# Kernel optimization log

Measured on AMD Instinct MI355X. Metric: run time of the kernel, lower is better.

The kernel has to match this reference:

```python
import jax, jax.numpy as jnp
import numpy as np

B, S, H, W, E, NH = 8, 16, 32, 32, 128, 8
HD = E // NH
EPS = 1e-5


def setup_inputs() -> dict:
    key = jax.random.key(0)
    ks = jax.random.split(key, 6)
    sc = lambda fan: 1.0 / np.sqrt(fan).astype(np.float32)
    return {
        "inputs": jax.random.normal(ks[0], (B, S, H, W, E), jnp.float32),
        "W_proj": jax.random.normal(ks[1], (E, E), jnp.float32) * sc(E),
        "ln_gamma": jnp.ones((E,), jnp.float32),
        "ln_beta": jnp.zeros((E,), jnp.float32),
        "W_in": jax.random.normal(ks[2], (E, 3 * E), jnp.float32) * sc(E),
        "W_out": jax.random.normal(ks[3], (E, E), jnp.float32) * sc(E),
        "conv_k": jax.random.normal(ks[4], (4 * E, 2 * E, 3, 3), jnp.float32) * sc(2 * E * 9),
    }


def reference(inputs, W_proj, ln_gamma, ln_beta, W_in, W_out, conv_k):
    # x = silu(project(inputs))
    x = jax.nn.silu(inputs @ W_proj)
    # LayerNorm over last dim
    mu = x.mean(-1, keepdims=True)
    var = x.var(-1, keepdims=True)
    x = (x - mu) * jax.lax.rsqrt(var + EPS) * ln_gamma + ln_beta
    # Multi-head attention over the sequence dim, batched over (b, h, w)
    qkv = (x @ W_in).reshape(B, S, H, W, NH, 3 * HD)
    q, k, v = jnp.split(qkv, 3, axis=-1)
    scale = 1.0 / np.sqrt(HD).astype(np.float32)
    scores = jnp.einsum('bshwid,blhwid->bhwisl', q, k) * scale  # (B,H,W,NH,S,S)
    tril = jnp.tril(jnp.ones((S, S), jnp.float32))
    # faithful to source: +1.0 on/below diagonal, -1000.0 above
    mask = tril * 1.0 + (1.0 - tril) * (-1000.0)
    attnw = jax.nn.softmax(scores + mask, axis=-1)
    ao = jnp.einsum('bhwisl,blhwid->bshwid', attnw, v).reshape(B, S, H, W, E)
    x = ao @ W_out + inputs  # residual
    # ConvLSTM over seq: (B,S,H,W,E) -> (S,B,E,H,W) for scan
    xc = jnp.transpose(x, (1, 0, 4, 2, 3))
    h0 = jnp.zeros((B, E, H, W), x.dtype)
    c0 = jnp.zeros((B, E, H, W), x.dtype)

    def step(carry, xt):
        h, c = carry
        comb = jnp.concatenate([xt, h], axis=1)  # (B, 2E, H, W)
        cc = jax.lax.conv_general_dilated(
            comb, conv_k, window_strides=(1, 1), padding='SAME',
            dimension_numbers=('NCHW', 'OIHW', 'NCHW'))
        ci, cf, co, cg = jnp.split(cc, 4, axis=1)
        c_next = jax.nn.sigmoid(cf) * c + jax.nn.sigmoid(ci) * jnp.tanh(cg)
        h_next = jax.nn.sigmoid(co) * jnp.tanh(c_next)
        return (h_next, c_next), h_next

    _, outs = jax.lax.scan(step, (h0, c0), xc)  # (S,B,E,H,W)
    return jnp.transpose(outs, (1, 0, 3, 4, 2))  # (B,S,H,W,E)
```

## Files before the change

### kernel.cpp

```cpp
#include <hip/hip_runtime.h>
#include <math.h>

#define B_  8
#define S_  16
#define H_  32
#define W_  32
#define E_  128
#define NH_ 8
#define HD_ 16
#define HW_ (H_*W_)
#define NTOK (B_*S_*H_*W_)

typedef __attribute__((ext_vector_type(8))) short short8;
typedef __attribute__((ext_vector_type(4))) short short4v;
typedef __attribute__((ext_vector_type(4))) float floatx4;

__device__ __forceinline__ float sigf(float x){
    return 1.f/(1.f+__expf(-x));
}
__device__ __forceinline__ float tanh_fast(float x){
    x = fminf(fmaxf(x, -15.f), 15.f);
    float e = __expf(2.f*x);
    return (e-1.f)/(e+1.f);
}
__device__ __forceinline__ unsigned short f2bf(float f){
    unsigned int u = __float_as_uint(f);
    u = (u + 0x7fffu + ((u >> 16) & 1u)) >> 16;
    return (unsigned short)u;
}
__device__ __forceinline__ float bf2f(unsigned short h){
    return __uint_as_float(((unsigned int)h) << 16);
}

__device__ __forceinline__ void st_gate(float* p, float v){ *p = v; }
__device__ __forceinline__ void st_gate(unsigned short* p, float v){ *p = f2bf(v); }
__device__ __forceinline__ void load_gate(const float* p, float* o){
    float4 v = *(const float4*)p; o[0]=v.x; o[1]=v.y; o[2]=v.z; o[3]=v.w;
}
__device__ __forceinline__ void load_gate(const unsigned short* p, float* o){
    ushort4 v = *(const ushort4*)p;
    o[0]=bf2f(v.x); o[1]=bf2f(v.y); o[2]=bf2f(v.z); o[3]=bf2f(v.w);
}

__global__ __launch_bounds__(256)
void k_pack_wproj(const float* __restrict__ Wp, short* __restrict__ Wpp){
    int p = blockIdx.x*256 + threadIdx.x;
    int L = p & 63;
    int idx = p >> 6;
    int nt = idx / 12, kb = idx - nt*12;
    int n = nt*16 + (L & 15);
    int kr = (kb & 3)*32 + (L >> 4)*8;
    bool lo = (kb >= 8);
    short8 v;
    #pragma unroll
    for (int j=0;j<8;j++){
        float wv = Wp[(kr+j)*128 + n];
        unsigned short h = f2bf(wv);
        v[j] = lo ? (short)f2bf(wv - bf2f(h)) : (short)h;
    }
    *(short8*)&Wpp[(long)p*8] = v;
}

__global__ __launch_bounds__(256,2)
void k_proj_ln_mfma(const float* __restrict__ in, const short* __restrict__ Wpp,
                    const float* __restrict__ gamma, const float* __restrict__ beta,
                    float* __restrict__ X){
    __shared__ short As[64*264];
    int tid = threadIdx.x;
    int w = tid >> 6, L = tid & 63;
    int quad = L >> 4, lm = L & 15;
    long r0 = (long)blockIdx.x * 64;

    {
        int c = (tid & 31)*4;
        int rbase = tid >> 5;
        #pragma unroll
        for (int rr=0; rr<8; rr++){
            int r = rr*8 + rbase;
            float4 v = *(const float4*)&in[(r0 + r)*128 + c];
            short4v hv, lv;
            unsigned short h;
            h = f2bf(v.x); hv[0]=(short)h; lv[0]=(short)f2bf(v.x - bf2f(h));
            h = f2bf(v.y); hv[1]=(short)h; lv[1]=(short)f2bf(v.y - bf2f(h));
            h = f2bf(v.z); hv[2]=(short)h; lv[2]=(short)f2bf(v.z - bf2f(h));
            h = f2bf(v.w); hv[3]=(short)h; lv[3]=(short)f2bf(v.w - bf2f(h));
            *(short4v*)&As[r*264 + c] = hv;
            *(short4v*)&As[r*264 + 128 + c] = lv;
        }
    }
    __syncthreads();

    floatx4 acc[8];
    #pragma unroll
    for (int nt=0;nt<8;nt++) acc[nt] = (floatx4){0.f,0.f,0.f,0.f};
    const short8* Bp8 = (const short8*)Wpp;
    int arow = (w*16 + lm)*264 + quad*8;
    #pragma unroll
    for (int kb=0; kb<12; kb++){
        int off = (kb<4) ? kb*32 : ((kb<8) ? 128+(kb-4)*32 : (kb-8)*32);
        short8 af = *(const short8*)&As[arow + off];
        #pragma unroll
        for (int nt=0;nt<8;nt++){
            short8 bf = Bp8[(nt*12+kb)*64 + L];
            acc[nt] = __builtin_amdgcn_mfma_f32_16x16x32_bf16(af, bf, acc[nt], 0,0,0);
        }
    }

    float g[8], bb[8];
    #pragma unroll
    for (int nt=0;nt<8;nt++){ g[nt]=gamma[nt*16+lm]; bb[nt]=beta[nt*16+lm]; }
    float s1[4]={0,0,0,0}, s2[4]={0,0,0,0};
    #pragma unroll
    for (int nt=0;nt<8;nt++)
        #pragma unroll
        for (int r=0;r<4;r++){
            float a = acc[nt][r];
            float si = a*sigf(a);
            acc[nt][r] = si;
            s1[r] += si; s2[r] += si*si;
        }
    #pragma unroll
    for (int d=1; d<16; d<<=1)
        #pragma unroll
        for (int r=0;r<4;r++){
            s1[r] += __shfl_xor(s1[r], d);
            s2[r] += __shfl_xor(s2[r], d);
        }
    float mu[4], rs[4];
    #pragma unroll
    for (int r=0;r<4;r++){
        mu[r] = s1[r]*(1.f/128.f);
        float var = s2[r]*(1.f/128.f) - mu[r]*mu[r];
        rs[r] = rsqrtf(var + 1e-5f);
    }
    #pragma unroll
    for (int nt=0;nt<8;nt++)
        #pragma unroll
        for (int r=0;r<4;r++){
            long row = r0 + w*16 + quad*4 + r;
            X[row*128 + nt*16 + lm] = (acc[nt][r]-mu[r])*rs[r]*g[nt] + bb[nt];
        }
}

__global__ __launch_bounds__(256)
void k_pack_win(const float* __restrict__ Win, short* __restrict__ Winp){
    int p = blockIdx.x*256 + threadIdx.x;
    int L = p & 63;
    int idx = p >> 6;
    int nt = idx >> 2, kc = idx & 3;
    int n = nt*16 + (L & 15);
    int k0 = kc*32 + (L >> 4)*8;
    short8 v;
    #pragma unroll
    for (int j=0;j<8;j++) v[j] = (short)f2bf(Win[(k0+j)*384 + n]);
    *(short8*)&Winp[(long)p*8] = v;
}

__global__ __launch_bounds__(256)
void k_pack_wout(const float* __restrict__ Wout, short* __restrict__ Woutp){
    int p = blockIdx.x*256 + threadIdx.x;
    int L = p & 63;
    int idx = p >> 6;
    int h = idx >> 3, nt = idx & 7;
    int n = nt*16 + (L & 15);
    int k0 = (L >> 4)*8;
    short8 v;
    #pragma unroll
    for (int j=0;j<8;j++){
        int k = k0 + j;
        v[j] = (k < 16) ? (short)f2bf(Wout[(h*16+k)*128 + n]) : (short)0;
    }
    *(short8*)&Woutp[(long)p*8] = v;
}

__global__ __launch_bounds__(256,5)
void k_attn_mfma(const float* __restrict__ X, const short* __restrict__ Winp,
                 const short* __restrict__ Woutp, const float* __restrict__ resid,
                 float* __restrict__ Y){
    __shared__ short lds[16000];
    const int XO=0;
    const int QO=8704;
    const int KO=10240;
    const int VO=11776;
    const int PO=12928;
    const int AOO=14464;
    int tid = threadIdx.x;
    int w = tid >> 6, L = tid & 63;
    int quad = L >> 4, lm = L & 15;
    int b = blockIdx.x >> 8, tile = blockIdx.x & 255;
    int hw0 = tile * 4;
    int hw = hw0 + w;

    {
        int cq = L & 31, rh = L >> 5;
        for (int p=0; p<8; p++){
            int m = w*16 + p*2 + rh;
            int s = m & 15;
            float4 v = *(const float4*)&X[((((long)b*16 + s)*1024) + hw)*128 + cq*4];
            short4v hv;
            hv[0]=(short)f2bf(v.x); hv[1]=(short)f2bf(v.y);
            hv[2]=(short)f2bf(v.z); hv[3]=(short)f2bf(v.w);
            *(short4v*)&lds[XO + m*136 + cq*4] = hv;
        }
    }

    floatx4 Oa[8];
    #pragma unroll
    for (int nt=0;nt<8;nt++) Oa[nt] = (floatx4){0.f,0.f,0.f,0.f};

    const floatx4 zc = (floatx4){0.f,0.f,0.f,0.f};
    const short8 z8 = {0,0,0,0,0,0,0,0};
    int m0 = w*16;

    for (int h=0; h<8; h++){
        floatx4 qacc[3];
        #pragma unroll
        for (int t=0;t<3;t++) qacc[t] = zc;
        #pragma unroll
        for (int kc=0;kc<4;kc++){
            short8 af = *(const short8*)&lds[XO + (m0+lm)*136 + kc*32 + quad*8];
            #pragma unroll
            for (int t=0;t<3;t++){
                int nt = 3*h + t;
                short8 bf = *(const short8*)&Winp[(long)((nt*4+kc)*64 + L)*8];
                qacc[t] = __builtin_amdgcn_mfma_f32_16x16x32_bf16(af, bf, qacc[t], 0,0,0);
            }
        }
        #pragma unroll
        for (int r=0;r<4;r++){
            lds[QO + (m0+quad*4+r)*24 + lm] = (short)f2bf(qacc[0][r]);
            lds[KO + (m0+quad*4+r)*24 + lm] = (short)f2bf(qacc[1][r]);
        }
        {
            short4v vv;
            #pragma unroll
            for (int r=0;r<4;r++) vv[r] = (short)f2bf(qacc[2][r]);
            *(short4v*)&lds[VO + lm*72 + m0 + quad*4] = vv;
        }

        {
            short8 qf = z8, kf = z8;
            if (quad < 2){
                qf = *(const short8*)&lds[QO + (m0+lm)*24 + quad*8];
                kf = *(const short8*)&lds[KO + (m0+lm)*24 + quad*8];
            }
            floatx4 scv = __builtin_amdgcn_mfma_f32_16x16x32_bf16(qf, kf, zc, 0,0,0);
            float pv[4], mr[4];
            #pragma unroll
            for (int r=0;r<4;r++){
                int si = quad*4 + r;
                pv[r] = scv[r]*0.25f + (lm <= si ? 1.0f : -1000.0f);
                mr[r] = pv[r];
            }
            #pragma unroll
            for (int d=1; d<16; d<<=1)
                #pragma unroll
                for (int r=0;r<4;r++) mr[r] = fmaxf(mr[r], __shfl_xor(mr[r], d));
            float ex[4], sm[4];
            #pragma unroll
            for (int r=0;r<4;r++){ ex[r] = __expf(pv[r]-mr[r]); sm[r] = ex[r]; }
            #pragma unroll
            for (int d=1; d<16; d<<=1)
                #pragma unroll
                for (int r=0;r<4;r++) sm[r] += __shfl_xor(sm[r], d);
            #pragma unroll
            for (int r=0;r<4;r++)
                lds[PO + (m0+quad*4+r)*24 + lm] = (short)f2bf(ex[r]/sm[r]);

            short8 pf = z8, vf = z8;
            if (quad < 2){
                pf = *(const short8*)&lds[PO + (m0+lm)*24 + quad*8];
                vf = *(const short8*)&lds[VO + lm*72 + m0 + quad*8];
            }
            floatx4 aov = __builtin_amdgcn_mfma_f32_16x16x32_bf16(pf, vf, zc, 0,0,0);
            #pragma unroll
            for (int r=0;r<4;r++)
                lds[AOO + (m0+quad*4+r)*24 + lm] = (short)f2bf(aov[r]);
        }

        {
            short8 aof = z8;
            if (quad < 2)
                aof = *(const short8*)&lds[AOO + (m0+lm)*24 + quad*8];
            #pragma unroll
            for (int nt=0;nt<8;nt++){
                short8 wf = *(const short8*)&Woutp[(long)((h*8+nt)*64 + L)*8];
                Oa[nt] = __builtin_amdgcn_mfma_f32_16x16x32_bf16(aof, wf, Oa[nt], 0,0,0);
            }
        }
    }

    #pragma unroll
    for (int nt=0;nt<8;nt++){
        int n = nt*16 + lm;
        #pragma unroll
        for (int r=0;r<4;r++){
            int s = quad*4 + r;
            long addr = (((long)b*16 + s)*1024 + hw)*128 + n;
            Y[addr] = Oa[nt][r] + resid[addr];
        }
    }
}

__global__ __launch_bounds__(256)
void k_pack_w(const float* __restrict__ ck, short* __restrict__ Bp){
    int p = blockIdx.x*256 + threadIdx.x;
    int L = p & 63;
    int nt = (p >> 6) & 31;
    int c32 = (p >> 11) & 7;
    int tap = p >> 14;
    int oc = nt*16 + (L & 15);
    int kq = L >> 4;
    short8 v;
    #pragma unroll
    for (int j=0;j<8;j++){
        int ic = c32*32 + kq*8 + j;
        v[j] = (short)f2bf(ck[(oc*256+ic)*9 + tap]);
    }
    *(short8*)&Bp[(long)p*8] = v;
}

__global__ __launch_bounds__(256)
void k_pack_x(const float* __restrict__ X, short* __restrict__ xh, int s, int zero_h){
    int idx = blockIdx.x*256 + threadIdx.x;
    int row = idx >> 4;
    int ch = (idx & 15) * 8;
    int b = row >> 10, hw = row & 1023;
    const float* src = X + (((long)(b*16+s)*1024 + hw)*128 + ch);
    float4 a = *(const float4*)src;
    float4 c = *(const float4*)(src+4);
    short8 v;
    v[0]=(short)f2bf(a.x); v[1]=(short)f2bf(a.y); v[2]=(short)f2bf(a.z); v[3]=(short)f2bf(a.w);
    v[4]=(short)f2bf(c.x); v[5]=(short)f2bf(c.y); v[6]=(short)f2bf(c.z); v[7]=(short)f2bf(c.w);
    *(short8*)&xh[(long)row*256 + ch] = v;
    if (zero_h){
        short8 z = {0,0,0,0,0,0,0,0};
        *(short8*)&xh[(long)row*256 + 128 + ch] = z;
    }
}

template<typename GT>
__global__ __launch_bounds__(512,2)
void k_conv_mfma(const short* __restrict__ xh, const short* __restrict__ Bp,
                 GT* __restrict__ gbuf){
    __shared__ short As[4*34*264];
    int tid = threadIdx.x;
    int Nblk = blockIdx.x & 1, g = blockIdx.x >> 1;
    int b = g >> 4, y0 = (g & 15)*2;
    int w = tid >> 6, L = tid & 63;
    int quad = L >> 4, lm = L & 15;
    int wm = w >> 2, wn = w & 3;
    int ntg = Nblk*16 + wn*4;

    const short8 z8 = {0,0,0,0,0,0,0,0};
    {
        short8 vs[9];
        #pragma unroll
        for (int i=0; i<9; i++){
            int pidx = i*512 + tid;
            short8 v = z8;
            if (pidx < 4352){
                int cb  = pidx & 31;
                int pos = pidx >> 5;
                int row = pos / 34;
                int xp  = pos - row*34;
                int yy = y0 - 1 + row, xx = xp - 1;
                if (yy>=0 && yy<32 && xx>=0 && xx<32)
                    v = *(const short8*)&xh[(((long)(b*32+yy)*32+xx)<<8) + cb*8];
            }
            vs[i] = v;
        }
        #pragma unroll
        for (int i=0; i<9; i++){
            int pidx = i*512 + tid;
            if (pidx < 4352){
                int cb  = pidx & 31;
                int pos = pidx >> 5;
                *(short8*)&As[pos*264 + cb*8] = vs[i];
            }
        }
    }
    __syncthreads();

    floatx4 acc[2][4];
    #pragma unroll
    for (int mtl=0;mtl<2;mtl++)
        #pragma unroll
        for (int nti=0;nti<4;nti++)
            acc[mtl][nti] = (floatx4){0.f,0.f,0.f,0.f};

    const short8* Bp8 = (const short8*)Bp;

    for (int tap=0; tap<9; tap++){
        int dy = tap/3 - 1, dx = tap - (tap/3)*3 - 1;
        int abase[2];
        #pragma unroll
        for (int mtl=0;mtl<2;mtl++){
            int x = mtl*16 + lm;
            abase[mtl] = (((wm+dy+1)*34) + x + dx + 1)*264 + quad*8;
        }
        #pragma unroll
        for (int sic=0; sic<4; sic++){
            #pragma unroll
            for (int c2=0; c2<2; c2++){
                short8 bfr[4];
                #pragma unroll
                for (int nti=0;nti<4;nti++)
                    bfr[nti] = Bp8[((tap*8 + sic*2 + c2)*32 + ntg + nti)*64 + L];
                #pragma unroll
                for (int mtl=0;mtl<2;mtl++){
                    short8 afr = *(const short8*)&As[abase[mtl] + sic*64 + c2*32];
                    #pragma unroll
                    for (int nti=0;nti<4;nti++)
                        acc[mtl][nti] = __builtin_amdgcn_mfma_f32_16x16x32_bf16(afr, bfr[nti], acc[mtl][nti], 0,0,0);
                }
            }
        }
    }

    #pragma unroll
    for (int mtl=0;mtl<2;mtl++){
        #pragma unroll
        for (int nti=0;nti<4;nti++){
            int n = Nblk*256 + (wn*4+nti)*16 + lm;
            #pragma unroll
            for (int r=0;r<4;r++){
                long row = (long)g*64 + (wm*2+mtl)*16 + quad*4 + r;
                st_gate(&gbuf[row*512 + n], acc[mtl][nti][r]);
            }
        }
    }
}

template<typename GT>
__global__ __launch_bounds__(256)
void k_lstm(const GT* __restrict__ gbuf, float* __restrict__ cbuf,
            float* __restrict__ X, short* __restrict__ xh, int s){
    int idx = blockIdx.x*256 + threadIdx.x;
    int row = idx >> 5;
    int c4 = (idx & 31)*4;
    float gi[4], gf[4], go[4], gg[4];
    const GT* gp = gbuf + (long)row*512 + c4;
    load_gate(gp,       gi);
    load_gate(gp + 128, gf);
    load_gate(gp + 256, go);
    load_gate(gp + 384, gg);
    float co[4];
    if (s == 0){ co[0]=co[1]=co[2]=co[3]=0.f; }
    else {
        float4 cv = *(const float4*)&cbuf[(long)row*128 + c4];
        co[0]=cv.x; co[1]=cv.y; co[2]=cv.z; co[3]=cv.w;
    }
    float cn[4], hn[4];
    #pragma unroll
    for (int j=0;j<4;j++){
        cn[j] = sigf(gf[j])*co[j] + sigf(gi[j])*tanh_fast(gg[j]);
        hn[j] = sigf(go[j])*tanh_fast(cn[j]);
    }
    *(float4*)&cbuf[(long)row*128 + c4] = make_float4(cn[0],cn[1],cn[2],cn[3]);
    int b = row >> 10, hw = row & 1023;
    long xoff = (((long)(b*16+s)*1024 + hw)*128) + c4;
    *(float4*)&X[xoff] = make_float4(hn[0],hn[1],hn[2],hn[3]);
    ushort4 hv;
    hv.x = f2bf(hn[0]); hv.y = f2bf(hn[1]); hv.z = f2bf(hn[2]); hv.w = f2bf(hn[3]);
    *(ushort4*)&xh[(long)row*256 + 128 + c4] = hv;
    if (s < 15){
        long x2 = (((long)(b*16+s+1)*1024 + hw)*128) + c4;
        float4 xv = *(const float4*)&X[x2];
        ushort4 xb;
        xb.x = f2bf(xv.x); xb.y = f2bf(xv.y); xb.z = f2bf(xv.z); xb.w = f2bf(xv.w);
        *(ushort4*)&xh[(long)row*256 + c4] = xb;
    }
}

extern "C" void kernel_launch(void* const* d_in, const int* in_sizes, int n_in,
                              void* d_out, int out_size, void* d_ws, size_t ws_size,
                              hipStream_t stream){
    const float* inputs = (const float*)d_in[0];
    const float* Wp     = (const float*)d_in[1];
    const float* gamma  = (const float*)d_in[2];
    const float* beta   = (const float*)d_in[3];
    const float* Win    = (const float*)d_in[4];
    const float* Wout   = (const float*)d_in[5];
    const float* ck     = (const float*)d_in[6];
    float* X = (float*)d_out;

    char* ws = (char*)d_ws;
    const size_t szB    = 147456ull*16;
    const size_t szXH   = 8192ull*256*2;
    const size_t szC    = 8192ull*128*4;
    const size_t szWin  = 6144ull*16;
    const size_t szWout = 4096ull*16;
    short* Bp    = (short*)(ws);
    short* xh    = (short*)(ws + szB);
    float* cbuf  = (float*)(ws + szB + szXH);
    short* Winp  = (short*)(ws + szB + szXH + szC);
    short* Woutp = (short*)(ws + szB + szXH + szC + szWin);
    char*  gch   =         ws + szB + szXH + szC + szWin + szWout;
    bool gate_f32 = ws_size >= (szB + szXH + szC + szWin + szWout + 8192ull*512*4);
    short* Wprojp = (short*)gch;

    k_pack_w<<<576, 256, 0, stream>>>(ck, Bp);
    k_pack_win<<<24, 256, 0, stream>>>(Win, Winp);
    k_pack_wout<<<16, 256, 0, stream>>>(Wout, Woutp);
    k_pack_wproj<<<24, 256, 0, stream>>>(Wp, Wprojp);
    k_proj_ln_mfma<<<NTOK/64, 256, 0, stream>>>(inputs, Wprojp, gamma, beta, X);
    k_attn_mfma<<<2048, 256, 0, stream>>>(X, Winp, Woutp, inputs, X);
    k_pack_x<<<512, 256, 0, stream>>>(X, xh, 0, 1);

    if (gate_f32){
        float* gbuf = (float*)gch;
        for (int s=0; s<16; s++){
            k_conv_mfma<float><<<256, 512, 0, stream>>>(xh, Bp, gbuf);
            k_lstm<float><<<1024, 256, 0, stream>>>(gbuf, cbuf, X, xh, s);
        }
    } else {
        unsigned short* gbuf = (unsigned short*)gch;
        for (int s=0; s<16; s++){
            k_conv_mfma<unsigned short><<<256, 512, 0, stream>>>(xh, Bp, gbuf);
            k_lstm<unsigned short><<<1024, 256, 0, stream>>>(gbuf, cbuf, X, xh, s);
        }
    }
}
```

Baseline: 871.4 us.

## Retile projection and attention kernels so each wave reuses weight fragments across row tiles

The projection+LayerNorm kernel now splits the output columns across waves instead of rows. Each wave loads 2 weight column tiles and reuses them across 4 row tiles, so the LayerNorm statistics need a cross-wave reduction through shared memory. The attention kernel now processes 8 spatial positions per block (2 per wave), so each weight fragment loaded from global serves two MFMAs. It also reuses the Q/K LDS regions for P/AO and halves the grid. This cuts redundant global weight loads at the cost of more registers, more LDS and lower occupancy (launch bounds change).

Result: no change. 863.6 us (-0.9%).

```diff
diff --git a/kernel.cpp b/kernel.cpp
--- a/kernel.cpp
+++ b/kernel.cpp
@@ -61,11 +61,12 @@
     *(short8*)&Wpp[(long)p*8] = v;
 }
 
-__global__ __launch_bounds__(256,2)
+__global__ __launch_bounds__(256,4)
 void k_proj_ln_mfma(const float* __restrict__ in, const short* __restrict__ Wpp,
                     const float* __restrict__ gamma, const float* __restrict__ beta,
                     float* __restrict__ X){
     __shared__ short As[64*264];
+    __shared__ float red[4][64][2];
     int tid = threadIdx.x;
     int w = tid >> 6, L = tid & 63;
     int quad = L >> 4, lm = L & 15;
@@ -90,56 +91,79 @@
     }
     __syncthreads();
 
-    floatx4 acc[8];
-    #pragma unroll
-    for (int nt=0;nt<8;nt++) acc[nt] = (floatx4){0.f,0.f,0.f,0.f};
+    floatx4 acc[4][2];
+    #pragma unroll
+    for (int mtl=0;mtl<4;mtl++)
+        #pragma unroll
+        for (int nti=0;nti<2;nti++)
+            acc[mtl][nti] = (floatx4){0.f,0.f,0.f,0.f};
     const short8* Bp8 = (const short8*)Wpp;
-    int arow = (w*16 + lm)*264 + quad*8;
     #pragma unroll
     for (int kb=0; kb<12; kb++){
         int off = (kb<4) ? kb*32 : ((kb<8) ? 128+(kb-4)*32 : (kb-8)*32);
-        short8 af = *(const short8*)&As[arow + off];
-        #pragma unroll
-        for (int nt=0;nt<8;nt++){
-            short8 bf = Bp8[(nt*12+kb)*64 + L];
-            acc[nt] = __builtin_amdgcn_mfma_f32_16x16x32_bf16(af, bf, acc[nt], 0,0,0);
-        }
-    }
-
-    float g[8], bb[8];
-    #pragma unroll
-    for (int nt=0;nt<8;nt++){ g[nt]=gamma[nt*16+lm]; bb[nt]=beta[nt*16+lm]; }
-    float s1[4]={0,0,0,0}, s2[4]={0,0,0,0};
-    #pragma unroll
-    for (int nt=0;nt<8;nt++)
+        short8 af[4];
+        #pragma unroll
+        for (int mtl=0;mtl<4;mtl++)
+            af[mtl] = *(const short8*)&As[(mtl*16+lm)*264 + off + quad*8];
+        #pragma unroll
+        for (int nti=0;nti<2;nti++){
+            short8 bf = Bp8[((2*w+nti)*12+kb)*64 + L];
+            #pragma unroll
+            for (int mtl=0;mtl<4;mtl++)
+                acc[mtl][nti] = __builtin_amdgcn_mfma_f32_16x16x32_bf16(af[mtl], bf, acc[mtl][nti], 0,0,0);
+        }
+    }
+
+    #pragma unroll
+    for (int mtl=0;mtl<4;mtl++){
+        float p1[4]={0,0,0,0}, p2[4]={0,0,0,0};
+        #pragma unroll
+        for (int nti=0;nti<2;nti++)
+            #pragma unroll
+            for (int r=0;r<4;r++){
+                float a = acc[mtl][nti][r];
+                float si = a*sigf(a);
+                acc[mtl][nti][r] = si;
+                p1[r] += si; p2[r] += si*si;
+            }
+        #pragma unroll
+        for (int d=1; d<16; d<<=1)
+            #pragma unroll
+            for (int r=0;r<4;r++){
+                p1[r] += __shfl_xor(p1[r], d);
+                p2[r] += __shfl_xor(p2[r], d);
+            }
+        if (lm == 0){
+            #pragma unroll
+            for (int r=0;r<4;r++){
+                int row = mtl*16 + quad*4 + r;
+                red[w][row][0] = p1[r];
+                red[w][row][1] = p2[r];
+            }
+        }
+    }
+    __syncthreads();
+    float g[2], bb[2];
+    #pragma unroll
+    for (int nti=0;nti<2;nti++){
+        g[nti]  = gamma[(2*w+nti)*16 + lm];
+        bb[nti] = beta [(2*w+nti)*16 + lm];
+    }
+    #pragma unroll
+    for (int mtl=0;mtl<4;mtl++){
         #pragma unroll
         for (int r=0;r<4;r++){
-            float a = acc[nt][r];
-            float si = a*sigf(a);
-            acc[nt][r] = si;
-            s1[r] += si; s2[r] += si*si;
-        }
-    #pragma unroll
-    for (int d=1; d<16; d<<=1)
-        #pragma unroll
-        for (int r=0;r<4;r++){
-            s1[r] += __shfl_xor(s1[r], d);
-            s2[r] += __shfl_xor(s2[r], d);
-        }
-    float mu[4], rs[4];
-    #pragma unroll
-    for (int r=0;r<4;r++){
-        mu[r] = s1[r]*(1.f/128.f);
-        float var = s2[r]*(1.f/128.f) - mu[r]*mu[r];
-        rs[r] = rsqrtf(var + 1e-5f);
-    }
-    #pragma unroll
-    for (int nt=0;nt<8;nt++)
-        #pragma unroll
-        for (int r=0;r<4;r++){
-            long row = r0 + w*16 + quad*4 + r;
-            X[row*128 + nt*16 + lm] = (acc[nt][r]-mu[r])*rs[r]*g[nt] + bb[nt];
-        }
+            int row = mtl*16 + quad*4 + r;
+            float s1 = red[0][row][0] + red[1][row][0] + red[2][row][0] + red[3][row][0];
+            float s2 = red[0][row][1] + red[1][row][1] + red[2][row][1] + red[3][row][1];
+            float mu  = s1 * (1.f/128.f);
+            float var = s2 * (1.f/128.f) - mu*mu;
+            float rs  = rsqrtf(var + 1e-5f);
+            #pragma unroll
+            for (int nti=0;nti<2;nti++)
+                X[(r0+row)*128 + (2*w+nti)*16 + lm] = (acc[mtl][nti][r]-mu)*rs*g[nti] + bb[nti];
+        }
+    }
 }
 
 __global__ __launch_bounds__(256)
@@ -173,30 +197,29 @@
     *(short8*)&Woutp[(long)p*8] = v;
 }
 
-__global__ __launch_bounds__(256,5)
+__global__ __launch_bounds__(256,2)
 void k_attn_mfma(const float* __restrict__ X, const short* __restrict__ Winp,
                  const short* __restrict__ Woutp, const float* __restrict__ resid,
                  float* __restrict__ Y){
-    __shared__ short lds[16000];
+    __shared__ short lds[25728];
     const int XO=0;
-    const int QO=8704;
-    const int KO=10240;
-    const int VO=11776;
-    const int PO=12928;
-    const int AOO=14464;
+    const int QO=17408;
+    const int KO=20480;
+    const int VO=23552;
+    const int PO=QO;
+    const int AOO=KO;
     int tid = threadIdx.x;
     int w = tid >> 6, L = tid & 63;
     int quad = L >> 4, lm = L & 15;
-    int b = blockIdx.x >> 8, tile = blockIdx.x & 255;
-    int hw0 = tile * 4;
-    int hw = hw0 + w;
+    int b = blockIdx.x >> 7, tile = blockIdx.x & 127;
+    int hw0 = tile * 8;
 
     {
         int cq = L & 31, rh = L >> 5;
-        for (int p=0; p<8; p++){
-            int m = w*16 + p*2 + rh;
-            int s = m & 15;
-            float4 v = *(const float4*)&X[((((long)b*16 + s)*1024) + hw)*128 + cq*4];
+        for (int p=0; p<16; p++){
+            int m = w*32 + p*2 + rh;
+            int s = m & 15, st = m >> 4;
+            float4 v = *(const float4*)&X[((((long)b*16 + s)*1024) + hw0 + st)*128 + cq*4];
             short4v hv;
             hv[0]=(short)f2bf(v.x); hv[1]=(short)f2bf(v.y);
             hv[2]=(short)f2bf(v.z); hv[3]=(short)f2bf(v.w);
@@ -204,45 +227,57 @@
         }
     }
 
-    floatx4 Oa[8];
-    #pragma unroll
-    for (int nt=0;nt<8;nt++) Oa[nt] = (floatx4){0.f,0.f,0.f,0.f};
+    floatx4 Oa[2][8];
+    #pragma unroll
+    for (int mt=0;mt<2;mt++)
+        #pragma unroll
+        for (int nt=0;nt<8;nt++) Oa[mt][nt] = (floatx4){0.f,0.f,0.f,0.f};
 
     const floatx4 zc = (floatx4){0.f,0.f,0.f,0.f};
     const short8 z8 = {0,0,0,0,0,0,0,0};
-    int m0 = w*16;
 
     for (int h=0; h<8; h++){
-        floatx4 qacc[3];
-        #pragma unroll
-        for (int t=0;t<3;t++) qacc[t] = zc;
+        floatx4 qacc[2][3];
+        #pragma unroll
+        for (int mt=0;mt<2;mt++)
+            #pragma unroll
+            for (int t=0;t<3;t++) qacc[mt][t] = zc;
         #pragma unroll
         for (int kc=0;kc<4;kc++){
-            short8 af = *(const short8*)&lds[XO + (m0+lm)*136 + kc*32 + quad*8];
+            short8 af[2];
+            #pragma unroll
+            for (int mt=0;mt<2;mt++)
+                af[mt] = *(const short8*)&lds[XO + (w*32+mt*16+lm)*136 + kc*32 + quad*8];
             #pragma unroll
             for (int t=0;t<3;t++){
                 int nt = 3*h + t;
                 short8 bf = *(const short8*)&Winp[(long)((nt*4+kc)*64 + L)*8];
-                qacc[t] = __builtin_amdgcn_mfma_f32_16x16x32_bf16(af, bf, qacc[t], 0,0,0);
-            }
-        }
-        #pragma unroll
-        for (int r=0;r<4;r++){
-            lds[QO + (m0+quad*4+r)*24 + lm] = (short)f2bf(qacc[0][r]);
-            lds[KO + (m0+quad*4+r)*24 + lm] = (short)f2bf(qacc[1][r]);
-        }
-        {
+                #pragma unroll
+                for (int mt=0;mt<2;mt++)
+                    qacc[mt][t] = __builtin_amdgcn_mfma_f32_16x16x32_bf16(af[mt], bf, qacc[mt][t], 0,0,0);
+            }
+        }
+        #pragma unroll
+        for (int mt=0;mt<2;mt++){
+            int m0 = w*32 + mt*16;
+            #pragma unroll
+            for (int r=0;r<4;r++){
+                lds[QO + (m0+quad*4+r)*24 + lm] = (short)f2bf(qacc[mt][0][r]);
+                lds[KO + (m0+quad*4+r)*24 + lm] = (short)f2bf(qacc[mt][1][r]);
+            }
             short4v vv;
             #pragma unroll
-            for (int r=0;r<4;r++) vv[r] = (short)f2bf(qacc[2][r]);
-            *(short4v*)&lds[VO + lm*72 + m0 + quad*4] = vv;
-        }
-
-        {
+            for (int r=0;r<4;r++) vv[r] = (short)f2bf(qacc[mt][2][r]);
+            *(short4v*)&lds[VO + lm*136 + m0 + quad*4] = vv;
+        }
+
+        #pragma unroll
+        for (int mt=0;mt<2;mt++){
+            int sb = w*32 + mt*16;
             short8 qf = z8, kf = z8;
             if (quad < 2){
-                qf = *(const short8*)&lds[QO + (m0+lm)*24 + quad*8];
-                kf = *(const short8*)&lds[KO + (m0+lm)*24 + quad*8];
+                qf = *(const short8*)&lds[QO + (sb+lm)*24 + quad*8];
+                kf = *(const short8*)&lds[KO + (sb+lm)*24 + quad*8];
             }
             floatx4 scv = __builtin_amdgcn_mfma_f32_16x16x32_bf16(qf, kf, zc, 0,0,0);
             float pv[4], mr[4];
@@ -265,39 +300,44 @@
                 for (int r=0;r<4;r++) sm[r] += __shfl_xor(sm[r], d);
             #pragma unroll
             for (int r=0;r<4;r++)
-                lds[PO + (m0+quad*4+r)*24 + lm] = (short)f2bf(ex[r]/sm[r]);
+                lds[PO + (sb+quad*4+r)*24 + lm] = (short)f2bf(ex[r]/sm[r]);
 
             short8 pf = z8, vf = z8;
             if (quad < 2){
-                pf = *(const short8*)&lds[PO + (m0+lm)*24 + quad*8];
-                vf = *(const short8*)&lds[VO + lm*72 + m0 + quad*8];
+                pf = *(const short8*)&lds[PO + (sb+lm)*24 + quad*8];
+                vf = *(const short8*)&lds[VO + lm*136 + sb + quad*8];
             }
             floatx4 aov = __builtin_amdgcn_mfma_f32_16x16x32_bf16(pf, vf, zc, 0,0,0);
             #pragma unroll
             for (int r=0;r<4;r++)
-                lds[AOO + (m0+quad*4+r)*24 + lm] = (short)f2bf(aov[r]);
-        }
-
-        {
+                lds[AOO + (sb+quad*4+r)*24 + lm] = (short)f2bf(aov[r]);
+        }
+
+        #pragma unroll
+        for (int mt=0;mt<2;mt++){
             short8 aof = z8;
             if (quad < 2)
-                aof = *(const short8*)&lds[AOO + (m0+lm)*24 + quad*8];
+                aof = *(const short8*)&lds[AOO + (w*32+mt*16+lm)*24 + quad*8];
             #pragma unroll
             for (int nt=0;nt<8;nt++){
                 short8 wf = *(const short8*)&Woutp[(long)((h*8+nt)*64 + L)*8];
-                Oa[nt] = __builtin_amdgcn_mfma_f32_16x16x32_bf16(aof, wf, Oa[nt], 0,0,0);
-            }
-        }
-    }
-
-    #pragma unroll
-    for (int nt=0;nt<8;nt++){
-        int n = nt*16 + lm;
-        #pragma unroll
-        for (int r=0;r<4;r++){
-            int s = quad*4 + r;
-            long addr = (((long)b*16 + s)*1024 + hw)*128 + n;
-            Y[addr] = Oa[nt][r] + resid[addr];
+                Oa[mt][nt] = __builtin_amdgcn_mfma_f32_16x16x32_bf16(aof, wf, Oa[mt][nt], 0,0,0);
+            }
+        }
+    }
+
+    #pragma unroll
+    for (int mt=0;mt<2;mt++){
+        int hw = hw0 + w*2 + mt;
+        #pragma unroll
+        for (int nt=0;nt<8;nt++){
+            int n = nt*16 + lm;
+            #pragma unroll
+            for (int r=0;r<4;r++){
+                int s = quad*4 + r;
+                long addr = (((long)b*16 + s)*1024 + hw)*128 + n;
+                Y[addr] = Oa[mt][nt][r] + resid[addr];
+            }
         }
     }
 }
@@ -505,7 +545,7 @@
     k_pack_wout<<<16, 256, 0, stream>>>(Wout, Woutp);
     k_pack_wproj<<<24, 256, 0, stream>>>(Wp, Wprojp);
     k_proj_ln_mfma<<<NTOK/64, 256, 0, stream>>>(inputs, Wprojp, gamma, beta, X);
-    k_attn_mfma<<<2048, 256, 0, stream>>>(X, Winp, Woutp, inputs, X);
+    k_attn_mfma<<<1024, 256, 0, stream>>>(X, Winp, Woutp, inputs, X);
     k_pack_x<<<512, 256, 0, stream>>>(X, xh, 0, 1);
 
     if (gate_f32){
```

## Retile projection-LN across warps and enlarge conv spatial tile to four rows

Applied to the files above, without the earlier changes.

In the projection + SiLU + LayerNorm kernel, each warp now covers all 64 rows but only two of the eight 16-column tiles. The per-row statistics are combined across warps through a small shared-memory reduction, and the occupancy hint rises to 4 blocks. In the ConvLSTM conv kernel, each block now covers four image rows instead of two and 128 output channels instead of 256. This cuts redundant halo loads per output row, but the shared tile grows to about 107 KB. That may prevent two blocks from sharing a CU and lower occupancy.

After: 859.7 us. Within noise of the previous version (-1.3%).

```diff
diff --git a/kernel.cpp b/kernel.cpp
--- a/kernel.cpp
+++ b/kernel.cpp
@@ -61,11 +61,12 @@
     *(short8*)&Wpp[(long)p*8] = v;
 }
 
-__global__ __launch_bounds__(256,2)
+__global__ __launch_bounds__(256,4)
 void k_proj_ln_mfma(const float* __restrict__ in, const short* __restrict__ Wpp,
                     const float* __restrict__ gamma, const float* __restrict__ beta,
                     float* __restrict__ X){
     __shared__ short As[64*264];
+    __shared__ float red[4][64][2];
     int tid = threadIdx.x;
     int w = tid >> 6, L = tid & 63;
     int quad = L >> 4, lm = L & 15;
@@ -90,56 +91,79 @@
     }
     __syncthreads();
 
-    floatx4 acc[8];
-    #pragma unroll
-    for (int nt=0;nt<8;nt++) acc[nt] = (floatx4){0.f,0.f,0.f,0.f};
+    floatx4 acc[4][2];
+    #pragma unroll
+    for (int mtl=0;mtl<4;mtl++)
+        #pragma unroll
+        for (int nti=0;nti<2;nti++)
+            acc[mtl][nti] = (floatx4){0.f,0.f,0.f,0.f};
     const short8* Bp8 = (const short8*)Wpp;
-    int arow = (w*16 + lm)*264 + quad*8;
     #pragma unroll
     for (int kb=0; kb<12; kb++){
         int off = (kb<4) ? kb*32 : ((kb<8) ? 128+(kb-4)*32 : (kb-8)*32);
-        short8 af = *(const short8*)&As[arow + off];
-        #pragma unroll
-        for (int nt=0;nt<8;nt++){
-            short8 bf = Bp8[(nt*12+kb)*64 + L];
-            acc[nt] = __builtin_amdgcn_mfma_f32_16x16x32_bf16(af, bf, acc[nt], 0,0,0);
-        }
-    }
-
-    float g[8], bb[8];
-    #pragma unroll
-    for (int nt=0;nt<8;nt++){ g[nt]=gamma[nt*16+lm]; bb[nt]=beta[nt*16+lm]; }
-    float s1[4]={0,0,0,0}, s2[4]={0,0,0,0};
-    #pragma unroll
-    for (int nt=0;nt<8;nt++)
+        short8 af[4];
+        #pragma unroll
+        for (int mtl=0;mtl<4;mtl++)
+            af[mtl] = *(const short8*)&As[(mtl*16+lm)*264 + off + quad*8];
+        #pragma unroll
+        for (int nti=0;nti<2;nti++){
+            short8 bf = Bp8[((2*w+nti)*12+kb)*64 + L];
+            #pragma unroll
+            for (int mtl=0;mtl<4;mtl++)
+                acc[mtl][nti] = __builtin_amdgcn_mfma_f32_16x16x32_bf16(af[mtl], bf, acc[mtl][nti], 0,0,0);
+        }
+    }
+
+    #pragma unroll
+    for (int mtl=0;mtl<4;mtl++){
+        float p1[4]={0,0,0,0}, p2[4]={0,0,0,0};
+        #pragma unroll
+        for (int nti=0;nti<2;nti++)
+            #pragma unroll
+            for (int r=0;r<4;r++){
+                float a = acc[mtl][nti][r];
+                float si = a*sigf(a);
+                acc[mtl][nti][r] = si;
+                p1[r] += si; p2[r] += si*si;
+            }
+        #pragma unroll
+        for (int d=1; d<16; d<<=1)
+            #pragma unroll
+            for (int r=0;r<4;r++){
+                p1[r] += __shfl_xor(p1[r], d);
+                p2[r] += __shfl_xor(p2[r], d);
+            }
+        if (lm == 0){
+            #pragma unroll
+            for (int r=0;r<4;r++){
+                int row = mtl*16 + quad*4 + r;
+                red[w][row][0] = p1[r];
+                red[w][row][1] = p2[r];
+            }
+        }
+    }
+    __syncthreads();
+    float g[2], bb[2];
+    #pragma unroll
+    for (int nti=0;nti<2;nti++){
+        g[nti]  = gamma[(2*w+nti)*16 + lm];
+        bb[nti] = beta [(2*w+nti)*16 + lm];
+    }
+    #pragma unroll
+    for (int mtl=0;mtl<4;mtl++){
         #pragma unroll
         for (int r=0;r<4;r++){
-            float a = acc[nt][r];
-            float si = a*sigf(a);
-            acc[nt][r] = si;
-            s1[r] += si; s2[r] += si*si;
-        }
-    #pragma unroll
-    for (int d=1; d<16; d<<=1)
-        #pragma unroll
-        for (int r=0;r<4;r++){
-            s1[r] += __shfl_xor(s1[r], d);
-            s2[r] += __shfl_xor(s2[r], d);
-        }
-    float mu[4], rs[4];
-    #pragma unroll
-    for (int r=0;r<4;r++){
-        mu[r] = s1[r]*(1.f/128.f);
-        float var = s2[r]*(1.f/128.f) - mu[r]*mu[r];
-        rs[r] = rsqrtf(var + 1e-5f);
-    }
-    #pragma unroll
-    for (int nt=0;nt<8;nt++)
-        #pragma unroll
-        for (int r=0;r<4;r++){
-            long row = r0 + w*16 + quad*4 + r;
-            X[row*128 + nt*16 + lm] = (acc[nt][r]-mu[r])*rs[r]*g[nt] + bb[nt];
-        }
+            int row = mtl*16 + quad*4 + r;
+            float s1 = red[0][row][0] + red[1][row][0] + red[2][row][0] + red[3][row][0];
+            float s2 = red[0][row][1] + red[1][row][1] + red[2][row][1] + red[3][row][1];
+            float mu  = s1 * (1.f/128.f);
+            float var = s2 * (1.f/128.f) - mu*mu;
+            float rs  = rsqrtf(var + 1e-5f);
+            #pragma unroll
+            for (int nti=0;nti<2;nti++)
+                X[(r0+row)*128 + (2*w+nti)*16 + lm] = (acc[mtl][nti][r]-mu)*rs*g[nti] + bb[nti];
+        }
+    }
 }
 
 __global__ __launch_bounds__(256)
@@ -343,23 +367,23 @@
 __global__ __launch_bounds__(512,2)
 void k_conv_mfma(const short* __restrict__ xh, const short* __restrict__ Bp,
                  GT* __restrict__ gbuf){
-    __shared__ short As[4*34*264];
+    __shared__ short As[6*34*264];
     int tid = threadIdx.x;
-    int Nblk = blockIdx.x & 1, g = blockIdx.x >> 1;
-    int b = g >> 4, y0 = (g & 15)*2;
+    int Nblk = blockIdx.x & 3, g = blockIdx.x >> 2;
+    int b = g >> 3, y0 = (g & 7)*4;
     int w = tid >> 6, L = tid & 63;
     int quad = L >> 4, lm = L & 15;
-    int wm = w >> 2, wn = w & 3;
-    int ntg = Nblk*16 + wn*4;
+    int wm = w >> 1, wn = w & 1;
+    int ntg = Nblk*8 + wn*4;
 
     const short8 z8 = {0,0,0,0,0,0,0,0};
     {
-        short8 vs[9];
-        #pragma unroll
-        for (int i=0; i<9; i++){
+        short8 vs[13];
+        #pragma unroll
+        for (int i=0; i<13; i++){
             int pidx = i*512 + tid;
             short8 v = z8;
-            if (pidx < 4352){
+            if (pidx < 6528){
                 int cb  = pidx & 31;
                 int pos = pidx >> 5;
                 int row = pos / 34;
@@ -371,9 +395,9 @@
             vs[i] = v;
         }
         #pragma unroll
-        for (int i=0; i<9; i++){
+        for (int i=0; i<13; i++){
             int pidx = i*512 + tid;
-            if (pidx < 4352){
+            if (pidx < 6528){
                 int cb  = pidx & 31;
                 int pos = pidx >> 5;
                 *(short8*)&As[pos*264 + cb*8] = vs[i];
@@ -422,10 +446,10 @@
     for (int mtl=0;mtl<2;mtl++){
         #pragma unroll
         for (int nti=0;nti<4;nti++){
-            int n = Nblk*256 + (wn*4+nti)*16 + lm;
+            int n = Nblk*128 + (wn*4+nti)*16 + lm;
             #pragma unroll
             for (int r=0;r<4;r++){
-                long row = (long)g*64 + (wm*2+mtl)*16 + quad*4 + r;
+                long row = (long)g*128 + wm*32 + mtl*16 + quad*4 + r;
                 st_gate(&gbuf[row*512 + n], acc[mtl][nti][r]);
             }
         }
```
